# Kernel optimization log

Hardware: AMD Instinct MI355X
Metric: run time of the kernel (lower is better)

The kernel has to match this reference:

```python
import jax, jax.numpy as jnp
import numpy as np

BLOCK = 64  # diagonal block size (matches block_size init kwarg)

def setup_inputs() -> dict:
    key = jax.random.key(0)
    k1, k2, k3, k4 = jax.random.split(key, 4)
    b, h, n, d, e = 2, 16, 8192, 64, 64
    query = jax.random.normal(k1, (b, h, n, d), dtype=jnp.float32)
    key_t = jax.random.normal(k2, (b, h, n, d), dtype=jnp.float32)
    value = jax.random.normal(k3, (b, h, n, e), dtype=jnp.float32)
    s = jax.random.uniform(k4, (h,), dtype=jnp.float32)  # per-head decay rate
    return {"query": query, "key": key_t, "value": value, "s": s}

def reference(query, key, value, s):
    # Lightning-attention diagonal-block decayed linear attention.
    # Only intra-block causal pairs contribute:
    #   O[i] = sum_{j<=i, same BLOCK} exp(-s*(i-j)) * (q_i . k_j) * v_j
    b, h, n, d = query.shape
    e = value.shape[-1]
    G = n // BLOCK  # n chosen as multiple of BLOCK
    q = query.reshape(b, h, G, BLOCK, d)
    k = key.reshape(b, h, G, BLOCK, d)
    v = value.reshape(b, h, G, BLOCK, e)
    idx = jnp.arange(BLOCK)
    diff = (idx[:, None] - idx[None, :]).astype(jnp.float32)  # [BLOCK, BLOCK]
    # decay[h,i,j] = exp(-s_h*(i-j)) for i>=j else 0 (causal within block)
    decay = jnp.where(diff >= 0, jnp.exp(-s[:, None, None] * diff), 0.0)
    qk = jnp.einsum('bhgid,bhgjd->bhgij', q, k) * decay[None, :, None]
    out = jnp.einsum('bhgij,bhgje->bhgie', qk, v)
    return out.reshape(b, h, n, e)
```

## Files before the change

### kernel.cpp

```cpp
#include <hip/hip_runtime.h>
#include <stdint.h>


#define H_   16
#define N_   8192
#define G_   (N_ / 64)
#define LDSP 72

typedef __attribute__((ext_vector_type(8))) short bf16x8;
typedef __attribute__((ext_vector_type(4))) float f32x4;

static __device__ __forceinline__ unsigned short f2bf(float x) {
    union { float f; uint32_t u; } un; un.f = x;
    uint32_t u = un.u;
    u += 0x7FFFu + ((u >> 16) & 1u);
    return (unsigned short)(u >> 16);
}

__global__ __launch_bounds__(256, 4)
void lightning_diag(const float* __restrict__ q,
                    const float* __restrict__ k,
                    const float* __restrict__ v,
                    const float* __restrict__ s,
                    float* __restrict__ out)
{
    __shared__ unsigned short Qs[64 * LDSP];
    __shared__ unsigned short Ks[64 * LDSP];
    __shared__ unsigned short Vt[64 * LDSP];
    __shared__ unsigned short Ss[4][16 * LDSP];

    const int tid  = threadIdx.x;
    const int wave = tid >> 6;
    const int lane = tid & 63;
    const int g16  = lane >> 4;
    const int l16  = lane & 15;

    const int    idx  = blockIdx.x;
    const int    hi   = (idx / G_) % H_;
    const size_t base = (size_t)idx * 4096;

    const float sh = s[hi];
    const float c  = -sh * 1.44269504088896f;

    {
        const float4* qg = (const float4*)(q + base);
        const float4* kg = (const float4*)(k + base);
        const float4* vg = (const float4*)(v + base);
        #pragma unroll
        for (int it = 0; it < 4; ++it) {
            const int fi  = tid + it * 256;
            const int row = fi >> 4;
            const int col = (fi & 15) << 2;
            float4 a  = qg[fi];
            float4 b  = kg[fi];
            float4 vv = vg[fi];
            ushort4 qa = make_ushort4(f2bf(a.x), f2bf(a.y), f2bf(a.z), f2bf(a.w));
            ushort4 ka = make_ushort4(f2bf(b.x), f2bf(b.y), f2bf(b.z), f2bf(b.w));
            *(ushort4*)&Qs[row * LDSP + col] = qa;
            *(ushort4*)&Ks[row * LDSP + col] = ka;
            Vt[(col + 0) * LDSP + row] = f2bf(vv.x);
            Vt[(col + 1) * LDSP + row] = f2bf(vv.y);
            Vt[(col + 2) * LDSP + row] = f2bf(vv.z);
            Vt[(col + 3) * LDSP + row] = f2bf(vv.w);
        }
    }
    __syncthreads();

    f32x4 acc[4];
    #pragma unroll
    for (int t = 0; t < 4; ++t) acc[t] = (f32x4){0.f, 0.f, 0.f, 0.f};

    const int arow = wave * 16 + l16;
    const bf16x8 a0 = *(const bf16x8*)&Qs[arow * LDSP + g16 * 8];
    const bf16x8 a1 = *(const bf16x8*)&Qs[arow * LDSP + g16 * 8 + 32];
    #pragma unroll
    for (int tc = 0; tc < 4; ++tc) {
        const int brow = tc * 16 + l16;
        const bf16x8 b0 = *(const bf16x8*)&Ks[brow * LDSP + g16 * 8];
        const bf16x8 b1 = *(const bf16x8*)&Ks[brow * LDSP + g16 * 8 + 32];
        acc[tc] = __builtin_amdgcn_mfma_f32_16x16x32_bf16(a0, b0, acc[tc], 0, 0, 0);
        acc[tc] = __builtin_amdgcn_mfma_f32_16x16x32_bf16(a1, b1, acc[tc], 0, 0, 0);
    }

    unsigned short* ss = Ss[wave];
    #pragma unroll
    for (int tc = 0; tc < 4; ++tc) {
        #pragma unroll
        for (int r = 0; r < 4; ++r) {
            const int il   = wave * 16 + g16 * 4 + r;
            const int jl   = tc * 16 + l16;
            const int diff = il - jl;
            const float f  = (diff >= 0) ? exp2f(c * (float)diff) : 0.0f;
            ss[(g16 * 4 + r) * LDSP + jl] = f2bf(acc[tc][r] * f);
        }
    }
    __syncthreads();

    f32x4 oacc[4];
    #pragma unroll
    for (int t = 0; t < 4; ++t) oacc[t] = (f32x4){0.f, 0.f, 0.f, 0.f};
    const bf16x8 sa0 = *(const bf16x8*)&ss[l16 * LDSP + g16 * 8];
    const bf16x8 sa1 = *(const bf16x8*)&ss[l16 * LDSP + g16 * 8 + 32];
    #pragma unroll
    for (int nc = 0; nc < 4; ++nc) {
        const int vrow = nc * 16 + l16;
        const bf16x8 b0 = *(const bf16x8*)&Vt[vrow * LDSP + g16 * 8];
        const bf16x8 b1 = *(const bf16x8*)&Vt[vrow * LDSP + g16 * 8 + 32];
        oacc[nc] = __builtin_amdgcn_mfma_f32_16x16x32_bf16(sa0, b0, oacc[nc], 0, 0, 0);
        oacc[nc] = __builtin_amdgcn_mfma_f32_16x16x32_bf16(sa1, b1, oacc[nc], 0, 0, 0);
    }

    float* og = out + base;
    #pragma unroll
    for (int nc = 0; nc < 4; ++nc) {
        #pragma unroll
        for (int r = 0; r < 4; ++r) {
            og[(wave * 16 + g16 * 4 + r) * 64 + nc * 16 + l16] = oacc[nc][r];
        }
    }
}

extern "C" void kernel_launch(void* const* d_in, const int* in_sizes, int n_in,
                              void* d_out, int out_size, void* d_ws, size_t ws_size,
                              hipStream_t stream) {
    const float* q = (const float*)d_in[0];
    const float* k = (const float*)d_in[1];
    const float* v = (const float*)d_in[2];
    const float* s = (const float*)d_in[3];
    float* out = (float*)d_out;
    const int grid = in_sizes[0] / 4096;
    lightning_diag<<<grid, 256, 0, stream>>>(q, k, v, s, out);
}
```

Before: 217.0 us.

## Process four tiles per block with register prefetch of next tile

Each block now handles four consecutive 64-row tiles, prefetching the next tile's Q/K/V into registers while the current tile computes. V is loaded in a row-interleaved order so the transpose into LDS uses vector ushort4 stores, the separate score buffer is dropped by reusing the Q LDS region, and the decay uses the hardware exp2 intrinsic. This is meant to hide global load latency and cut launch and LDS costs, at the price of more registers and a grid four times smaller (4096 tiles become 1024 blocks), which may reduce occupancy.

```diff
diff --git a/kernel.cpp b/kernel.cpp
--- a/kernel.cpp
+++ b/kernel.cpp
@@ -6,15 +6,22 @@
 #define N_   8192
 #define G_   (N_ / 64)
 #define LDSP 72
+#define TPB  4
 
 typedef __attribute__((ext_vector_type(8))) short bf16x8;
 typedef __attribute__((ext_vector_type(4))) float f32x4;
+
+union F4 { float4 v; float f[4]; };
 
 static __device__ __forceinline__ unsigned short f2bf(float x) {
     union { float f; uint32_t u; } un; un.f = x;
     uint32_t u = un.u;
     u += 0x7FFFu + ((u >> 16) & 1u);
     return (unsigned short)(u >> 16);
+}
+
+static __device__ __forceinline__ ushort4 cvt4(float4 a) {
+    return make_ushort4(f2bf(a.x), f2bf(a.y), f2bf(a.z), f2bf(a.w));
 }
 
 __global__ __launch_bounds__(256, 4)
@@ -27,96 +34,124 @@
     __shared__ unsigned short Qs[64 * LDSP];
     __shared__ unsigned short Ks[64 * LDSP];
     __shared__ unsigned short Vt[64 * LDSP];
-    __shared__ unsigned short Ss[4][16 * LDSP];
 
     const int tid  = threadIdx.x;
     const int wave = tid >> 6;
     const int lane = tid & 63;
     const int g16  = lane >> 4;
     const int l16  = lane & 15;
+    const int rq   = tid >> 4;
+    const int cq   = tid & 15;
 
-    const int    idx  = blockIdx.x;
-    const int    hi   = (idx / G_) % H_;
-    const size_t base = (size_t)idx * 4096;
+    const int    t0    = blockIdx.x * TPB;
+    const int    hi    = (t0 / G_) % H_;
+    const size_t base0 = (size_t)t0 * 4096;
 
-    const float sh = s[hi];
-    const float c  = -sh * 1.44269504088896f;
+    const float c = -s[hi] * 1.44269504088896f;
 
+    F4 pq[4], pk[4], pv[4];
     {
-        const float4* qg = (const float4*)(q + base);
-        const float4* kg = (const float4*)(k + base);
-        const float4* vg = (const float4*)(v + base);
+        const float4* qg = (const float4*)(q + base0);
+        const float4* kg = (const float4*)(k + base0);
+        const float4* vg = (const float4*)(v + base0);
+        #pragma unroll
+        for (int it = 0; it < 4; ++it) {
+            const int fi = tid + it * 256;
+            pq[it].v = qg[fi];
+            pk[it].v = kg[fi];
+            pv[it].v = vg[(4 * rq + it) * 16 + cq];
+        }
+    }
+
+    #pragma unroll
+    for (int t = 0; t < TPB; ++t) {
+        const size_t base = base0 + (size_t)t * 4096;
+
         #pragma unroll
         for (int it = 0; it < 4; ++it) {
             const int fi  = tid + it * 256;
             const int row = fi >> 4;
             const int col = (fi & 15) << 2;
-            float4 a  = qg[fi];
-            float4 b  = kg[fi];
-            float4 vv = vg[fi];
-            ushort4 qa = make_ushort4(f2bf(a.x), f2bf(a.y), f2bf(a.z), f2bf(a.w));
-            ushort4 ka = make_ushort4(f2bf(b.x), f2bf(b.y), f2bf(b.z), f2bf(b.w));
-            *(ushort4*)&Qs[row * LDSP + col] = qa;
-            *(ushort4*)&Ks[row * LDSP + col] = ka;
-            Vt[(col + 0) * LDSP + row] = f2bf(vv.x);
-            Vt[(col + 1) * LDSP + row] = f2bf(vv.y);
-            Vt[(col + 2) * LDSP + row] = f2bf(vv.z);
-            Vt[(col + 3) * LDSP + row] = f2bf(vv.w);
+            *(ushort4*)&Qs[row * LDSP + col] = cvt4(pq[it].v);
+            *(ushort4*)&Ks[row * LDSP + col] = cvt4(pk[it].v);
         }
-    }
-    __syncthreads();
+        #pragma unroll
+        for (int j = 0; j < 4; ++j) {
+            ushort4 w = make_ushort4(f2bf(pv[0].f[j]), f2bf(pv[1].f[j]),
+                                     f2bf(pv[2].f[j]), f2bf(pv[3].f[j]));
+            *(ushort4*)&Vt[(4 * cq + j) * LDSP + 4 * rq] = w;
+        }
 
-    f32x4 acc[4];
-    #pragma unroll
-    for (int t = 0; t < 4; ++t) acc[t] = (f32x4){0.f, 0.f, 0.f, 0.f};
+        if (t + 1 < TPB) {
+            const size_t nb = base + 4096;
+            const float4* qn = (const float4*)(q + nb);
+            const float4* kn = (const float4*)(k + nb);
+            const float4* vn = (const float4*)(v + nb);
+            #pragma unroll
+            for (int it = 0; it < 4; ++it) {
+                const int fi = tid + it * 256;
+                pq[it].v = qn[fi];
+                pk[it].v = kn[fi];
+                pv[it].v = vn[(4 * rq + it) * 16 + cq];
+            }
+        }
 
-    const int arow = wave * 16 + l16;
-    const bf16x8 a0 = *(const bf16x8*)&Qs[arow * LDSP + g16 * 8];
-    const bf16x8 a1 = *(const bf16x8*)&Qs[arow * LDSP + g16 * 8 + 32];
-    #pragma unroll
-    for (int tc = 0; tc < 4; ++tc) {
-        const int brow = tc * 16 + l16;
-        const bf16x8 b0 = *(const bf16x8*)&Ks[brow * LDSP + g16 * 8];
-        const bf16x8 b1 = *(const bf16x8*)&Ks[brow * LDSP + g16 * 8 + 32];
-        acc[tc] = __builtin_amdgcn_mfma_f32_16x16x32_bf16(a0, b0, acc[tc], 0, 0, 0);
-        acc[tc] = __builtin_amdgcn_mfma_f32_16x16x32_bf16(a1, b1, acc[tc], 0, 0, 0);
-    }
+        __syncthreads();
 
-    unsigned short* ss = Ss[wave];
-    #pragma unroll
-    for (int tc = 0; tc < 4; ++tc) {
+        f32x4 acc[4];
         #pragma unroll
-        for (int r = 0; r < 4; ++r) {
-            const int il   = wave * 16 + g16 * 4 + r;
-            const int jl   = tc * 16 + l16;
-            const int diff = il - jl;
-            const float f  = (diff >= 0) ? exp2f(c * (float)diff) : 0.0f;
-            ss[(g16 * 4 + r) * LDSP + jl] = f2bf(acc[tc][r] * f);
+        for (int tt = 0; tt < 4; ++tt) acc[tt] = (f32x4){0.f, 0.f, 0.f, 0.f};
+
+        const int arow = wave * 16 + l16;
+        const bf16x8 a0 = *(const bf16x8*)&Qs[arow * LDSP + g16 * 8];
+        const bf16x8 a1 = *(const bf16x8*)&Qs[arow * LDSP + g16 * 8 + 32];
+        #pragma unroll
+        for (int tc = 0; tc < 4; ++tc) {
+            const int brow = tc * 16 + l16;
+            const bf16x8 b0 = *(const bf16x8*)&Ks[brow * LDSP + g16 * 8];
+            const bf16x8 b1 = *(const bf16x8*)&Ks[brow * LDSP + g16 * 8 + 32];
+            acc[tc] = __builtin_amdgcn_mfma_f32_16x16x32_bf16(a0, b0, acc[tc], 0, 0, 0);
+            acc[tc] = __builtin_amdgcn_mfma_f32_16x16x32_bf16(a1, b1, acc[tc], 0, 0, 0);
         }
-    }
-    __syncthreads();
 
-    f32x4 oacc[4];
-    #pragma unroll
-    for (int t = 0; t < 4; ++t) oacc[t] = (f32x4){0.f, 0.f, 0.f, 0.f};
-    const bf16x8 sa0 = *(const bf16x8*)&ss[l16 * LDSP + g16 * 8];
-    const bf16x8 sa1 = *(const bf16x8*)&ss[l16 * LDSP + g16 * 8 + 32];
-    #pragma unroll
-    for (int nc = 0; nc < 4; ++nc) {
-        const int vrow = nc * 16 + l16;
-        const bf16x8 b0 = *(const bf16x8*)&Vt[vrow * LDSP + g16 * 8];
-        const bf16x8 b1 = *(const bf16x8*)&Vt[vrow * LDSP + g16 * 8 + 32];
-        oacc[nc] = __builtin_amdgcn_mfma_f32_16x16x32_bf16(sa0, b0, oacc[nc], 0, 0, 0);
-        oacc[nc] = __builtin_amdgcn_mfma_f32_16x16x32_bf16(sa1, b1, oacc[nc], 0, 0, 0);
-    }
+        unsigned short* ss = &Qs[wave * 16 * LDSP];
+        #pragma unroll
+        for (int tc = 0; tc < 4; ++tc) {
+            #pragma unroll
+            for (int r = 0; r < 4; ++r) {
+                const int il   = wave * 16 + g16 * 4 + r;
+                const int jl   = tc * 16 + l16;
+                const int diff = il - jl;
+                const float f  = (diff >= 0)
+                               ? __builtin_amdgcn_exp2f(c * (float)diff) : 0.0f;
+                ss[(g16 * 4 + r) * LDSP + jl] = f2bf(acc[tc][r] * f);
+            }
+        }
 
-    float* og = out + base;
-    #pragma unroll
-    for (int nc = 0; nc < 4; ++nc) {
+        f32x4 oacc[4];
         #pragma unroll
-        for (int r = 0; r < 4; ++r) {
-            og[(wave * 16 + g16 * 4 + r) * 64 + nc * 16 + l16] = oacc[nc][r];
+        for (int tt = 0; tt < 4; ++tt) oacc[tt] = (f32x4){0.f, 0.f, 0.f, 0.f};
+        const bf16x8 sa0 = *(const bf16x8*)&ss[l16 * LDSP + g16 * 8];
+        const bf16x8 sa1 = *(const bf16x8*)&ss[l16 * LDSP + g16 * 8 + 32];
+        #pragma unroll
+        for (int nc = 0; nc < 4; ++nc) {
+            const int vrow = nc * 16 + l16;
+            const bf16x8 b0 = *(const bf16x8*)&Vt[vrow * LDSP + g16 * 8];
+            const bf16x8 b1 = *(const bf16x8*)&Vt[vrow * LDSP + g16 * 8 + 32];
+            oacc[nc] = __builtin_amdgcn_mfma_f32_16x16x32_bf16(sa0, b0, oacc[nc], 0, 0, 0);
+            oacc[nc] = __builtin_amdgcn_mfma_f32_16x16x32_bf16(sa1, b1, oacc[nc], 0, 0, 0);
         }
+
+        float* og = out + base;
+        #pragma unroll
+        for (int nc = 0; nc < 4; ++nc) {
+            #pragma unroll
+            for (int r = 0; r < 4; ++r) {
+                og[(wave * 16 + g16 * 4 + r) * 64 + nc * 16 + l16] = oacc[nc][r];
+            }
+        }
+
+        if (t + 1 < TPB) __syncthreads();
     }
 }
 
@@ -128,6 +163,6 @@
     const float* v = (const float*)d_in[2];
     const float* s = (const float*)d_in[3];
     float* out = (float*)d_out;
-    const int grid = in_sizes[0] / 4096;
-    lightning_diag<<<grid, 256, 0, stream>>>(q, k, v, s, out);
+    const int tiles = in_sizes[0] / 4096;
+    lightning_diag<<<tiles / TPB, 256, 0, stream>>>(q, k, v, s, out);
 }
```

Result: slower. 222.9 us (+2.7%).
